# Kernel tuning notes

Hardware: AMD Instinct MI355X
Metric: run time of the kernel (lower is better)

## Reference

```python
import jax, jax.numpy as jnp
import numpy as np
from functools import partial

C_IN = 32
KT = 10  # 3*3 taps + bias


def avgpool(x, k):
    B, C, H, W = x.shape
    return x.reshape(B, C, H // k, k, W // k, k).mean(axis=(3, 5))


def conv3x3(x, w, b):
    out = jax.lax.conv_general_dilated(
        x, w, window_strides=(1, 1), padding=[(1, 1), (1, 1)],
        dimension_numbers=("NCHW", "OIHW", "NCHW"))
    return out + b[None, :, None, None]


def conv1x1(x, w, b):
    # w: [O, C, 1, 1]
    return jnp.einsum("bchw,oc->bohw", x, w[:, :, 0, 0]) + b[None, :, None, None]


def predictor(x, w1, b1, w2, b2):
    return x + conv3x3(jax.nn.leaky_relu(conv3x3(x, w1, b1), 0.01), w2, b2)


def flying_conv(x, weight, bias):
    # x: [B,C,H,W]; weight: [B,C,Hb,Wb,9]; bias: [B,C,Hb,Wb]; 8x8 blocks
    B, C, H, W = x.shape
    Hb, Wb = H // 8, W // 8
    xp = jnp.pad(x, ((0, 0), (0, 0), (1, 1), (1, 1)))
    out = jnp.broadcast_to(bias[:, :, :, None, :, None], (B, C, Hb, 8, Wb, 8))
    for k in range(9):
        di, dj = k // 3, k % 3
        xs = xp[:, :, di:di + H, dj:dj + W].reshape(B, C, Hb, 8, Wb, 8)
        out = out + xs * weight[:, :, :, None, :, None, k]
    return out.reshape(B, C, H, W)


def setup_inputs() -> dict:
    key = jax.random.key(0)
    ks = jax.random.split(key, 5)
    B, C, H, W = 4, C_IN, 512, 512
    x = jax.random.normal(ks[0], (B, C, H, W), dtype=jnp.float32)
    pa_w = jax.random.normal(ks[1], (4, 2, C, C, 3, 3), dtype=jnp.float32) * 0.05
    pa_b = jnp.zeros((4, 2, C), dtype=jnp.float32)
    exp_w = jax.random.normal(ks[2], (C * KT, C, 1, 1), dtype=jnp.float32) * 0.05
    exp_b = jnp.zeros((C * KT,), dtype=jnp.float32)
    pw_w = jax.random.normal(ks[3], (C, C, 1, 1), dtype=jnp.float32) * 0.1
    pw_b = jnp.zeros((C,), dtype=jnp.float32)
    return {"x": x, "pa_w": pa_w, "pa_b": pa_b, "exp_w": exp_w,
            "exp_b": exp_b, "pw_w": pw_w, "pw_b": pw_b}


def reference(x, pa_w, pa_b, exp_w, exp_b, pw_w, pw_b):
    B, C, H, W = x.shape
    feat = avgpool(x, 4)  # H/4
    for i in range(4):
        feat = predictor(feat, pa_w[i, 0], pa_b[i, 0], pa_w[i, 1], pa_b[i, 1])
        if i == 1:
            feat = avgpool(feat, 2)  # -> H/8
    wmap = conv1x1(feat, exp_w, exp_b)  # [B, C*10, Hb, Wb]
    Hb, Wb = H // 8, W // 8
    wmap = jnp.tanh(wmap.reshape(B, C, KT, Hb, Wb).transpose(0, 1, 3, 4, 2))
    weight, bias = wmap[..., :9], wmap[..., 9]
    out = flying_conv(x, weight, bias)
    return conv1x1(out, pw_w, pw_b)
```

## Files before the change

### kernel.cpp

```cpp
#include <hip/hip_runtime.h>


#define BATCH 4
#define NCH 32
#define CS128 17680
#define SP128 136
#define CS64 4752
#define SP64 72

__device__ __forceinline__ float fast_tanh(float s) {
  float e = __expf(2.f * s);
  return fmaf(-2.f, __builtin_amdgcn_rcpf(e + 1.f), 1.f);
}

__global__ void zero_kernel(float* __restrict__ p) {
  int i = blockIdx.x * 256 + threadIdx.x;
  *reinterpret_cast<float4*>(p + (size_t)i * 4) = make_float4(0.f, 0.f, 0.f, 0.f);
}

__global__ void prep_kernel(const float* __restrict__ pa_w, const float* __restrict__ exp_w,
                            const float* __restrict__ pw_w, float* __restrict__ wt,
                            float* __restrict__ ewt, float* __restrict__ pwt) {
  int i = blockIdx.x * 256 + threadIdx.x;
  if (i < 73728) {
    int tap = i % 9; int t = i / 9;
    int ci = t & 31; t >>= 5;
    int co = t & 31; int layer = t >> 5;
    wt[((layer * 32 + ci) * 9 + tap) * 32 + co] = pa_w[i];
  } else if (i < 83968) {
    int j = i - 73728; int ci = j & 31; int o = j >> 5;
    ewt[ci * 320 + o] = exp_w[j];
  } else if (i < 84992) {
    int j = i - 83968; int c = j & 31; int o = j >> 5;
    pwt[c * 32 + o] = pw_w[j];
  }
}

__global__ void avgpool4_kernel(const float* __restrict__ x, float* __restrict__ outp) {
  int idx = blockIdx.x * 256 + threadIdx.x;
  if (idx >= BATCH * NCH * 128 * 128) return;
  int ow = idx & 127; int t = idx >> 7; int oh = t & 127; int bc = t >> 7;
  const float* src = x + ((size_t)(bc * 512 + oh * 4)) * 512 + ow * 4;
  float s = 0.f;
#pragma unroll
  for (int r = 0; r < 4; r++) {
    float4 v = *reinterpret_cast<const float4*>(src + (size_t)r * 512);
    s += v.x + v.y + v.z + v.w;
  }
  outp[(size_t)bc * CS128 + (size_t)(oh + 1) * SP128 + ow + 4] = s * 0.0625f;
}

__global__ void avgpool2_kernel(const float* __restrict__ inp, float* __restrict__ outp) {
  int idx = blockIdx.x * 256 + threadIdx.x;
  if (idx >= BATCH * NCH * 64 * 64) return;
  int ow = idx & 63; int t = idx >> 6; int oh = t & 63; int bc = t >> 6;
  const float* sp = inp + (size_t)bc * CS128 + (size_t)(2 * oh + 1) * SP128 + 2 * ow + 4;
  float2 a = *reinterpret_cast<const float2*>(sp);
  float2 b = *reinterpret_cast<const float2*>(sp + SP128);
  outp[(size_t)bc * CS64 + (size_t)(oh + 1) * SP64 + ow + 4] = (a.x + a.y + b.x + b.y) * 0.25f;
}

template <int HS, int SP, int CS, int NCO, bool RELU, bool RES>
__global__ __launch_bounds__(256) void conv3x3v_kernel(
    const float* __restrict__ in, const float* __restrict__ wt,
    const float* __restrict__ bias, const float* __restrict__ res,
    float* __restrict__ out) {
  constexpr int TX = HS / 16;
  constexpr int TY = HS / 32;
  constexpr int GROUPS = 32 / NCO;
  __shared__ float s_wt[288 * NCO];
  int blk = blockIdx.x;
  int g = blk % GROUPS; int rest = blk / GROUPS;
  int b = rest / (TX * TY); int t = rest % (TX * TY);
  int ty = t / TX, tx = t % TX;
  int og = g * NCO;
  int tid = threadIdx.x;

  for (int i = tid; i < 288 * NCO; i += 256) {
    int pos = i / NCO, o = i - pos * NCO;
    s_wt[i] = wt[pos * 32 + og + o];
  }
  __syncthreads();

  int px = tid & 15, py = tid >> 4;
  int gy = ty * 32 + py * 2, gx = tx * 16 + px;
  size_t pix = (size_t)(gy + 1) * SP + gx + 4;
  const float* inb = in + (size_t)b * 32 * CS + pix;

  float acc0[NCO], acc1[NCO];
#pragma unroll
  for (int o = 0; o < NCO; o++) { acc0[o] = bias[og + o]; acc1[o] = acc0[o]; }

#pragma unroll 2
  for (int ci = 0; ci < 32; ci++) {
    const float* p = inb + (size_t)ci * CS;
    float v[12];
    v[0] = p[-SP - 1];    v[1] = p[-SP];     v[2] = p[-SP + 1];
    v[3] = p[-1];         v[4] = p[0];       v[5] = p[1];
    v[6] = p[SP - 1];     v[7] = p[SP];      v[8] = p[SP + 1];
    v[9] = p[2 * SP - 1]; v[10] = p[2 * SP]; v[11] = p[2 * SP + 1];
    const float* wr = s_wt + ci * 9 * NCO;
#pragma unroll
    for (int tap = 0; tap < 9; tap++) {
      const float* wrow = wr + tap * NCO;
#pragma unroll
      for (int o = 0; o < NCO; o++) {
        float wv = wrow[o];
        acc0[o] = fmaf(v[tap], wv, acc0[o]);
        acc1[o] = fmaf(v[tap + 3], wv, acc1[o]);
      }
    }
  }

  float* ob = out + (size_t)b * 32 * CS + (size_t)og * CS + pix;
  const float* rb = RES ? (res + (size_t)b * 32 * CS + (size_t)og * CS + pix) : nullptr;
#pragma unroll
  for (int o = 0; o < NCO; o++) {
    float r0 = acc0[o], r1 = acc1[o];
    if (RELU) { r0 = r0 > 0.f ? r0 : 0.01f * r0; r1 = r1 > 0.f ? r1 : 0.01f * r1; }
    if (RES) { r0 += rb[(size_t)o * CS]; r1 += rb[(size_t)o * CS + SP]; }
    ob[(size_t)o * CS] = r0;
    ob[(size_t)o * CS + SP] = r1;
  }
}

template <int HS, int SP, int CS, int NCO, bool RELU, bool RES>
__global__ __launch_bounds__(256) void conv3x3d_kernel(
    const float* __restrict__ in, const float* __restrict__ wt,
    const float* __restrict__ bias, const float* __restrict__ res,
    float* __restrict__ out) {
  constexpr int TILES = HS / 16;
  constexpr int GROUPS = 32 / NCO;
  __shared__ float s_wt[288 * NCO];
  int blk = blockIdx.x;
  int g = blk % GROUPS; int rest = blk / GROUPS;
  int b = rest / (TILES * TILES); int t = rest % (TILES * TILES);
  int ty = t / TILES, tx = t % TILES;
  int og = g * NCO;
  int tid = threadIdx.x;

  for (int i = tid; i < 288 * NCO; i += 256) {
    int pos = i / NCO, o = i - pos * NCO;
    s_wt[i] = wt[pos * 32 + og + o];
  }
  __syncthreads();

  int px = tid & 15, py = tid >> 4;
  int gy = ty * 16 + py, gx = tx * 16 + px;
  size_t pix = (size_t)(gy + 1) * SP + gx + 4;
  const float* inb = in + (size_t)b * 32 * CS + pix;

  float acc[NCO];
#pragma unroll
  for (int o = 0; o < NCO; o++) acc[o] = bias[og + o];

#pragma unroll 2
  for (int ci = 0; ci < 32; ci++) {
    const float* p = inb + (size_t)ci * CS;
    float v[9];
    v[0] = p[-SP - 1]; v[1] = p[-SP]; v[2] = p[-SP + 1];
    v[3] = p[-1];      v[4] = p[0];   v[5] = p[1];
    v[6] = p[SP - 1];  v[7] = p[SP];  v[8] = p[SP + 1];
    const float* wr = s_wt + ci * 9 * NCO;
#pragma unroll
    for (int tap = 0; tap < 9; tap++) {
      const float* wrow = wr + tap * NCO;
#pragma unroll
      for (int o = 0; o < NCO; o++)
        acc[o] = fmaf(v[tap], wrow[o], acc[o]);
    }
  }

  float* ob = out + (size_t)b * 32 * CS + (size_t)og * CS + pix;
  const float* rb = RES ? (res + (size_t)b * 32 * CS + (size_t)og * CS + pix) : nullptr;
#pragma unroll
  for (int o = 0; o < NCO; o++) {
    float r2 = acc[o];
    if (RELU) r2 = r2 > 0.f ? r2 : 0.01f * r2;
    if (RES) r2 += rb[(size_t)o * CS];
    ob[(size_t)o * CS] = r2;
  }
}

__global__ __launch_bounds__(256) void expander_kernel(
    const float* __restrict__ feat, const float* __restrict__ ewt,
    const float* __restrict__ eb, float* __restrict__ wmap) {
  int idx = blockIdx.x * 256 + threadIdx.x;
  int wq = idx & 15; int t = idx >> 4;
  int o = t % 320; int rest = t / 320;
  int hb = rest & 63; int b = rest >> 6;
  const float* fp = feat + (size_t)b * 32 * CS64 + (size_t)(hb + 1) * SP64 + 4 + wq * 4;
  float s0 = eb[o];
  float s1 = s0, s2 = s0, s3 = s0;
#pragma unroll 8
  for (int ci = 0; ci < 32; ci++) {
    float4 f = *reinterpret_cast<const float4*>(fp + (size_t)ci * CS64);
    float wv = ewt[ci * 320 + o];
    s0 = fmaf(f.x, wv, s0); s1 = fmaf(f.y, wv, s1);
    s2 = fmaf(f.z, wv, s2); s3 = fmaf(f.w, wv, s3);
  }
  float4 r;
  r.x = fast_tanh(s0); r.y = fast_tanh(s1);
  r.z = fast_tanh(s2); r.w = fast_tanh(s3);
  *reinterpret_cast<float4*>(wmap + (size_t)((b * 64 + hb) * 320 + o) * 64 + wq * 4) = r;
}

__global__ __launch_bounds__(256) void fused_fly_pw_kernel(
    const float* __restrict__ x, const float* __restrict__ wmap,
    const float* __restrict__ pwt, const float* __restrict__ pw_b,
    float* __restrict__ out) {
  __shared__ float s_w[8][322];
  int blk = blockIdx.x;
  int wtile = blk & 7; int t = blk >> 3; int hb = t & 63; int b = t >> 6;
  int tid = threadIdx.x;

  const float* wsrc = wmap + (size_t)(b * 64 + hb) * 320 * 64 + wtile * 8;
#pragma unroll
  for (int j = 0; j < 10; j++) {
    int idx = j * 256 + tid;
    int tap = idx >> 3, wb8 = idx & 7;
    s_w[wb8][tap] = wsrc[(size_t)tap * 64 + wb8];
  }
  __syncthreads();

  int p = tid & 31, row = tid >> 5;
  int h = hb * 8 + row;
  int w0 = wtile * 64 + 2 * p;
  int wbl = p >> 2;
  const float* xb = x + (size_t)b * 32 * 262144;
  bool l4_ok = (w0 >= 4);
  bool wl_ok = (w0 > 0);
  bool m4_ok = (w0 < 510);

  float2 acc[32];
#pragma unroll
  for (int o = 0; o < 32; o++) {
    float bv = pw_b[o];
    acc[o].x = bv; acc[o].y = bv;
  }

  for (int c = 0; c < 32; c++) {
    const float2* w2p = reinterpret_cast<const float2*>(&s_w[wbl][c * 10]);
    float2 w01 = w2p[0], w23 = w2p[1], w45 = w2p[2], w67 = w2p[3], w89 = w2p[4];
    float wv[9];
    wv[0] = w01.x; wv[1] = w01.y; wv[2] = w23.x;
    wv[3] = w23.y; wv[4] = w45.x; wv[5] = w45.y;
    wv[6] = w67.x; wv[7] = w67.y; wv[8] = w89.x;
    float fly0 = w89.y, fly1 = w89.y;

    const float* xc = xb + (size_t)c * 262144;
#pragma unroll
    for (int di = 0; di < 3; di++) {
      int hh = h + di - 1;
      if (hh < 0 || hh >= 512) continue;
      const float* rp = xc + (size_t)hh * 512 + w0;
      float lv;
      if (l4_ok) {
        float4 L = *reinterpret_cast<const float4*>(rp - 4);
        lv = L.w;
      } else {
        lv = wl_ok ? rp[-1] : 0.f;
      }
      float4 M;
      if (m4_ok) {
        M = *reinterpret_cast<const float4*>(rp);
      } else {
        float2 tm = *reinterpret_cast<const float2*>(rp);
        M = make_float4(tm.x, tm.y, 0.f, 0.f);
      }
      float wa = wv[di * 3 + 0], wb_ = wv[di * 3 + 1], wc = wv[di * 3 + 2];
      fly0 = fmaf(lv,  wa, fly0); fly0 = fmaf(M.x, wb_, fly0); fly0 = fmaf(M.y, wc, fly0);
      fly1 = fmaf(M.x, wa, fly1); fly1 = fmaf(M.y, wb_, fly1); fly1 = fmaf(M.z, wc, fly1);
    }
    const float* prow = pwt + c * 32;
#pragma unroll
    for (int o = 0; o < 32; o++) {
      float pw = prow[o];
      acc[o].x = fmaf(fly0, pw, acc[o].x);
      acc[o].y = fmaf(fly1, pw, acc[o].y);
    }
  }
  float* ob = out + (size_t)b * 32 * 262144 + (size_t)h * 512 + w0;
#pragma unroll
  for (int o = 0; o < 32; o++)
    *reinterpret_cast<float2*>(ob + (size_t)o * 262144) = acc[o];
}

extern "C" void kernel_launch(void* const* d_in, const int* in_sizes, int n_in,
                              void* d_out, int out_size, void* d_ws, size_t ws_size,
                              hipStream_t stream) {
  const float* x     = (const float*)d_in[0];
  const float* pa_w  = (const float*)d_in[1];
  const float* pa_b  = (const float*)d_in[2];
  const float* exp_w = (const float*)d_in[3];
  const float* exp_b = (const float*)d_in[4];
  const float* pw_w  = (const float*)d_in[5];
  const float* pw_b  = (const float*)d_in[6];
  float* out = (float*)d_out;
  float* ws  = (float*)d_ws;

  float* feat0p = ws;
  float* tmpAp  = feat0p + 2263040;
  float* feat1p = tmpAp + 2263040;
  float* wmap   = feat1p + 608256;
  float* tmpBp  = wmap;
  float* wt     = wmap + 5242880;
  float* ewt    = wt + 73728;
  float* pwt    = ewt + 10240;

  hipLaunchKernelGGL(zero_kernel, dim3(5608), dim3(256), 0, stream, ws);
  hipLaunchKernelGGL(prep_kernel, dim3(332), dim3(256), 0, stream, pa_w, exp_w, pw_w, wt, ewt, pwt);
  hipLaunchKernelGGL(avgpool4_kernel, dim3(8192), dim3(256), 0, stream, x, feat0p);

  for (int i = 0; i < 2; i++) {
    const float* w1 = wt + (size_t)(i * 2 + 0) * 9216;
    const float* b1 = pa_b + (i * 2 + 0) * 32;
    const float* w2 = wt + (size_t)(i * 2 + 1) * 9216;
    const float* b2 = pa_b + (i * 2 + 1) * 32;
    hipLaunchKernelGGL((conv3x3v_kernel<128, SP128, CS128, 4, true, false>),
                       dim3(1024), dim3(256), 0, stream, feat0p, w1, b1, nullptr, tmpAp);
    hipLaunchKernelGGL((conv3x3v_kernel<128, SP128, CS128, 4, false, true>),
                       dim3(1024), dim3(256), 0, stream, tmpAp, w2, b2, feat0p, feat0p);
  }

  hipLaunchKernelGGL(avgpool2_kernel, dim3(2048), dim3(256), 0, stream, feat0p, feat1p);

  for (int i = 2; i < 4; i++) {
    const float* w1 = wt + (size_t)(i * 2 + 0) * 9216;
    const float* b1 = pa_b + (i * 2 + 0) * 32;
    const float* w2 = wt + (size_t)(i * 2 + 1) * 9216;
    const float* b2 = pa_b + (i * 2 + 1) * 32;
    hipLaunchKernelGGL((conv3x3d_kernel<64, SP64, CS64, 2, true, false>),
                       dim3(1024), dim3(256), 0, stream, feat1p, w1, b1, nullptr, tmpBp);
    hipLaunchKernelGGL((conv3x3d_kernel<64, SP64, CS64, 2, false, true>),
                       dim3(1024), dim3(256), 0, stream, tmpBp, w2, b2, feat1p, feat1p);
  }

  hipLaunchKernelGGL(expander_kernel, dim3(5120), dim3(256), 0, stream, feat1p, ewt, exp_b, wmap);

  hipLaunchKernelGGL(fused_fly_pw_kernel, dim3(2048), dim3(256), 0, stream,
                     x, wmap, pwt, pw_b, out);
}
```

Measured before the change: 338.0 us.

## Compute four horizontal pixels per thread in 3x3 conv and split fly kernel per batch

The 128-resolution 3x3 conv now assigns each thread a row of four adjacent pixels loaded with float4 reads, halving output channels per block to keep the grid size. This aims to cut redundant scalar global loads and vectorize stores. The final fused flying-conv/pointwise kernel is launched once per batch image instead of once for all, adding launch overhead and smaller grids, possibly to improve cache locality.

New measurement: 457.9 us. 35.5% more time.

```diff
diff --git a/kernel.cpp b/kernel.cpp
--- a/kernel.cpp
+++ b/kernel.cpp
@@ -61,11 +61,11 @@
 }
 
 template <int HS, int SP, int CS, int NCO, bool RELU, bool RES>
-__global__ __launch_bounds__(256) void conv3x3v_kernel(
+__global__ __launch_bounds__(256) void conv3x3h_kernel(
     const float* __restrict__ in, const float* __restrict__ wt,
     const float* __restrict__ bias, const float* __restrict__ res,
     float* __restrict__ out) {
-  constexpr int TX = HS / 16;
+  constexpr int TX = HS / 32;
   constexpr int TY = HS / 32;
   constexpr int GROUPS = 32 / NCO;
   __shared__ float s_wt[288 * NCO];
@@ -82,45 +82,63 @@
   }
   __syncthreads();
 
-  int px = tid & 15, py = tid >> 4;
-  int gy = ty * 32 + py * 2, gx = tx * 16 + px;
+  int qx = tid & 7, py = tid >> 3;
+  int gy = ty * 32 + py, gx = tx * 32 + qx * 4;
   size_t pix = (size_t)(gy + 1) * SP + gx + 4;
   const float* inb = in + (size_t)b * 32 * CS + pix;
 
-  float acc0[NCO], acc1[NCO];
-#pragma unroll
-  for (int o = 0; o < NCO; o++) { acc0[o] = bias[og + o]; acc1[o] = acc0[o]; }
+  float acc[4][NCO];
+#pragma unroll
+  for (int j = 0; j < 4; j++)
+#pragma unroll
+    for (int o = 0; o < NCO; o++) acc[j][o] = bias[og + o];
 
 #pragma unroll 2
   for (int ci = 0; ci < 32; ci++) {
     const float* p = inb + (size_t)ci * CS;
-    float v[12];
-    v[0] = p[-SP - 1];    v[1] = p[-SP];     v[2] = p[-SP + 1];
-    v[3] = p[-1];         v[4] = p[0];       v[5] = p[1];
-    v[6] = p[SP - 1];     v[7] = p[SP];      v[8] = p[SP + 1];
-    v[9] = p[2 * SP - 1]; v[10] = p[2 * SP]; v[11] = p[2 * SP + 1];
+    float v[3][6];
+#pragma unroll
+    for (int r = 0; r < 3; r++) {
+      const float* rp = p + (r - 1) * SP;
+      float4 L = *reinterpret_cast<const float4*>(rp - 4);
+      float4 M = *reinterpret_cast<const float4*>(rp);
+      float4 R = *reinterpret_cast<const float4*>(rp + 4);
+      v[r][0] = L.w; v[r][1] = M.x; v[r][2] = M.y;
+      v[r][3] = M.z; v[r][4] = M.w; v[r][5] = R.x;
+    }
     const float* wr = s_wt + ci * 9 * NCO;
 #pragma unroll
-    for (int tap = 0; tap < 9; tap++) {
-      const float* wrow = wr + tap * NCO;
-#pragma unroll
-      for (int o = 0; o < NCO; o++) {
-        float wv = wrow[o];
-        acc0[o] = fmaf(v[tap], wv, acc0[o]);
-        acc1[o] = fmaf(v[tap + 3], wv, acc1[o]);
+    for (int di = 0; di < 3; di++)
+#pragma unroll
+      for (int dj = 0; dj < 3; dj++) {
+        const float* wrow = wr + (di * 3 + dj) * NCO;
+#pragma unroll
+        for (int o = 0; o < NCO; o++) {
+          float wv = wrow[o];
+#pragma unroll
+          for (int j = 0; j < 4; j++)
+            acc[j][o] = fmaf(v[di][j + dj], wv, acc[j][o]);
+        }
       }
-    }
   }
 
   float* ob = out + (size_t)b * 32 * CS + (size_t)og * CS + pix;
   const float* rb = RES ? (res + (size_t)b * 32 * CS + (size_t)og * CS + pix) : nullptr;
 #pragma unroll
   for (int o = 0; o < NCO; o++) {
-    float r0 = acc0[o], r1 = acc1[o];
-    if (RELU) { r0 = r0 > 0.f ? r0 : 0.01f * r0; r1 = r1 > 0.f ? r1 : 0.01f * r1; }
-    if (RES) { r0 += rb[(size_t)o * CS]; r1 += rb[(size_t)o * CS + SP]; }
-    ob[(size_t)o * CS] = r0;
-    ob[(size_t)o * CS + SP] = r1;
+    float4 r4;
+    float* rr = &r4.x;
+#pragma unroll
+    for (int j = 0; j < 4; j++) {
+      float r2 = acc[j][o];
+      if (RELU) r2 = r2 > 0.f ? r2 : 0.01f * r2;
+      rr[j] = r2;
+    }
+    if (RES) {
+      float4 rv = *reinterpret_cast<const float4*>(rb + (size_t)o * CS);
+      r4.x += rv.x; r4.y += rv.y; r4.z += rv.z; r4.w += rv.w;
+    }
+    *reinterpret_cast<float4*>(ob + (size_t)o * CS) = r4;
   }
 }
 
@@ -208,10 +226,10 @@
 __global__ __launch_bounds__(256) void fused_fly_pw_kernel(
     const float* __restrict__ x, const float* __restrict__ wmap,
     const float* __restrict__ pwt, const float* __restrict__ pw_b,
-    float* __restrict__ out) {
+    float* __restrict__ out, int b0) {
   __shared__ float s_w[8][322];
   int blk = blockIdx.x;
-  int wtile = blk & 7; int t = blk >> 3; int hb = t & 63; int b = t >> 6;
+  int wtile = blk & 7; int hb = blk >> 3; int b = b0;
   int tid = threadIdx.x;
 
   const float* wsrc = wmap + (size_t)(b * 64 + hb) * 320 * 64 + wtile * 8;
@@ -317,9 +335,9 @@
     const float* b1 = pa_b + (i * 2 + 0) * 32;
     const float* w2 = wt + (size_t)(i * 2 + 1) * 9216;
     const float* b2 = pa_b + (i * 2 + 1) * 32;
-    hipLaunchKernelGGL((conv3x3v_kernel<128, SP128, CS128, 4, true, false>),
+    hipLaunchKernelGGL((conv3x3h_kernel<128, SP128, CS128, 2, true, false>),
                        dim3(1024), dim3(256), 0, stream, feat0p, w1, b1, nullptr, tmpAp);
-    hipLaunchKernelGGL((conv3x3v_kernel<128, SP128, CS128, 4, false, true>),
+    hipLaunchKernelGGL((conv3x3h_kernel<128, SP128, CS128, 2, false, true>),
                        dim3(1024), dim3(256), 0, stream, tmpAp, w2, b2, feat0p, feat0p);
   }
 
@@ -338,6 +356,7 @@
 
   hipLaunchKernelGGL(expander_kernel, dim3(5120), dim3(256), 0, stream, feat1p, ewt, exp_b, wmap);
 
-  hipLaunchKernelGGL(fused_fly_pw_kernel, dim3(2048), dim3(256), 0, stream,
-                     x, wmap, pwt, pw_b, out);
-}
+  for (int b0 = 0; b0 < 4; b0++)
+    hipLaunchKernelGGL(fused_fly_pw_kernel, dim3(512), dim3(256), 0, stream,
+                       x, wmap, pwt, pw_b, out, b0);
+}
```
